# Optimization experiments

Hardware: AMD Instinct MI355X
Metric: run time of the kernel (lower is better)

## Reference

```python
import jax, jax.numpy as jnp
import numpy as np
from jax import lax

DN = ("NCDHW", "OIDHW", "NCDHW")


def bn(x, g, b, eps=1e-5):
    # torch BatchNorm3d training-mode forward: biased batch stats over (N, *, spatial)
    axes = (0,) + tuple(range(2, x.ndim))
    m = x.mean(axes, keepdims=True)
    v = x.var(axes, keepdims=True)
    shp = (1, -1) + (1,) * (x.ndim - 2)
    return (x - m) * lax.rsqrt(v + eps) * g.reshape(shp) + b.reshape(shp)


def conv_bn_relu(x, w, g, b, stride=(1, 1, 1), pad=(1, 0, 0)):
    y = lax.conv_general_dilated(x, w, stride, [(p, p) for p in pad], dimension_numbers=DN)
    return jax.nn.relu(bn(y, g, b))


def pw_bn_relu(x, w, g, b):  # 1x1x1 conv (no bias) + BN + ReLU on (B,C,T,H,W)
    y = jnp.einsum('oi,bithw->bothw', w, x)
    return jax.nn.relu(bn(y, g, b))


def pam_enc(x, pe_w, pe_g, pe_b):
    b, c, t, h, w = x.shape
    xm = x.mean(axis=2)  # all adaptive pools have T_out = 1
    feats = []
    for i, s in enumerate((1, 2, 3, 6)):  # H,W chosen divisible by 1,2,3,6 -> exact block means
        p = xm.reshape(b, c, s, h // s, s, w // s).mean(axis=(3, 5))  # (B,C,s,s)
        f = jnp.einsum('oi,bihw->bohw', pe_w[i], p)
        f = jax.nn.relu(bn(f, pe_g[i], pe_b[i]))
        feats.append(f.reshape(b, c, s * s))
    return jnp.concatenate(feats, axis=2)  # (B, C, 1+4+9+36=50)


def pam_dec(x, y, wq, bq, wk, bk, wv, bv, scale):
    # x: (B,C,T,H,W), y: (B,K,C)
    b, c, t, h, w = x.shape
    n = t * h * w
    q = jnp.einsum('oi,bithw->bothw', wq, x) + bq.reshape(1, -1, 1, 1, 1)
    q = q.reshape(b, c // 4, n).transpose(0, 2, 1)            # (B,N,C/4)
    k = y @ wk.T + bk                                         # (B,K,C/4)
    attn = jax.nn.softmax(jnp.einsum('bnd,bkd->bnk', q, k), axis=-1)
    v = y @ wv.T + bv                                         # (B,K,C)
    out = jnp.einsum('bkc,bnk->bcn', v, attn).reshape(b, c, t, h, w)
    return scale * out + x


def cam_dec(x, y, scale):
    b, c, t, h, w = x.shape
    xf = x.reshape(b, c, -1)
    yf = y.reshape(b, y.shape[1], -1)
    energy = jnp.einsum('bcn,bkn->bck', xf, yf)               # (B,C,K)
    attn = jax.nn.softmax(energy.max(-1, keepdims=True) - energy, axis=-1)
    out = jnp.einsum('bck,bkn->bcn', attn, yf).reshape(b, c, t, h, w)
    return x + scale * out


def tam_dec(x, y, scale):
    xp = x.transpose(0, 2, 1, 3, 4)  # (B,T,C,H,W)
    yp = y.transpose(0, 2, 1, 3, 4)
    b, t, c, h, w = xp.shape
    xf = xp.reshape(b, t, -1)
    yf = yp.reshape(b, t, -1)
    energy = jnp.einsum('bim,bjm->bij', xf, yf)               # (B,T,T)
    attn = jax.nn.softmax(energy.max(-1, keepdims=True) - energy, axis=-1)
    out = jnp.einsum('bij,bjm->bim', attn, yf).reshape(b, t, c, h, w)
    return (xp + scale * out).transpose(0, 2, 1, 3, 4)


def caf(x1, x2, w_conv1, g_conv1, b_conv1, w_conv2, g_conv2, b_conv2, w_tam, g_tam, b_tam, w_cat, g_cat, b_cat, pe_w, pe_g, pe_b, pd_wq, pd_bq, pd_wk, pd_bk, pd_wv, pd_bv, pd_scale, ce_w, ce_g, ce_b, cd_scale, te_w, te_g, te_b, td_scale):
    c1 = lambda z: conv_bn_relu(z, w_conv1, g_conv1, b_conv1)
    c2 = lambda z: conv_bn_relu(z, w_conv2, g_conv2, b_conv2)
    x1i = c1(x1)  # conv1(x1) is used by both PAM and CAM branches (identical in torch)
    x2i = c1(x2)
    # PAM branches
    x1_pa = c2(pam_dec(x1i, pam_enc(x1i, pe_w, pe_g, pe_b).transpose(0, 2, 1), pd_wq, pd_bq, pd_wk, pd_bk, pd_wv, pd_bv, pd_scale))
    x2_pa = c2(pam_dec(x2i, pam_enc(x2i, pe_w, pe_g, pe_b).transpose(0, 2, 1), pd_wq, pd_bq, pd_wk, pd_bk, pd_wv, pd_bv, pd_scale))
    # CAM branches
    x1_ca = c2(cam_dec(x1i, pw_bn_relu(x1i, ce_w, ce_g, ce_b), cd_scale))
    x2_ca = c2(cam_dec(x2i, pw_bn_relu(x2i, ce_w, ce_g, ce_b), cd_scale))
    # TAM branch over temporal concat (2T frames)
    xt1 = c1(jnp.concatenate([x1, x2], axis=2))
    xt2 = pw_bn_relu(xt1, te_w, te_g, te_b)
    x_ta = conv_bn_relu(tam_dec(xt1, xt2, td_scale), w_tam, g_tam, b_tam, stride=(2, 1, 1))
    out1 = conv_bn_relu(jnp.concatenate([x1_pa, x2_ca, x_ta], axis=1), w_cat, g_cat, b_cat)
    out2 = conv_bn_relu(jnp.concatenate([x2_pa, x1_ca, x_ta], axis=1), w_cat, g_cat, b_cat)
    return out1, out2


def setup_inputs() -> dict:
    key = jax.random.key(0)
    B, C, T, H, W = 4, 256, 16, 36, 36
    IC = C // 4
    ks = iter(jax.random.split(key, 24))
    rn = lambda shape, s=0.05: jax.random.normal(next(ks), shape, jnp.float32) * s
    ones = lambda n: jnp.ones((n,), jnp.float32)
    zeros = lambda n: jnp.zeros((n,), jnp.float32)
    return {
        "x1": rn((B, C, T, H, W), 1.0),
        "x2": rn((B, C, T, H, W), 1.0),
        "w_conv1": rn((IC, C, 3, 1, 1)), "g_conv1": ones(IC), "b_conv1": zeros(IC),
        "w_conv2": rn((IC, IC, 3, 1, 1)), "g_conv2": ones(IC), "b_conv2": zeros(IC),
        "w_tam": rn((IC, IC, 3, 1, 1)), "g_tam": ones(IC), "b_tam": zeros(IC),
        "w_cat": rn((C, 3 * IC, 3, 1, 1)), "g_cat": ones(C), "b_cat": zeros(C),
        "pe_w": rn((4, IC, IC)), "pe_g": jnp.ones((4, IC), jnp.float32), "pe_b": jnp.zeros((4, IC), jnp.float32),
        "pd_wq": rn((IC // 4, IC)), "pd_bq": zeros(IC // 4),
        "pd_wk": rn((IC // 4, IC)), "pd_bk": zeros(IC // 4),
        "pd_wv": rn((IC, IC)), "pd_bv": zeros(IC),
        "pd_scale": jnp.full((1,), 0.1, jnp.float32),
        "ce_w": rn((IC // 16, IC)), "ce_g": ones(IC // 16), "ce_b": zeros(IC // 16),
        "cd_scale": jnp.full((1,), 0.1, jnp.float32),
        "te_w": rn((IC, IC)), "te_g": ones(IC), "te_b": zeros(IC),
        "td_scale": jnp.full((1,), 0.1, jnp.float32),
    }


def reference(x1, x2, w_conv1, g_conv1, b_conv1, w_conv2, g_conv2, b_conv2, w_tam, g_tam, b_tam, w_cat, g_cat, b_cat, pe_w, pe_g, pe_b, pd_wq, pd_bq, pd_wk, pd_bk, pd_wv, pd_bv, pd_scale, ce_w, ce_g, ce_b, cd_scale, te_w, te_g, te_b, td_scale):
    return caf(x1, x2, w_conv1, g_conv1, b_conv1, w_conv2, g_conv2, b_conv2, w_tam, g_tam, b_tam, w_cat, g_cat, b_cat, pe_w, pe_g, pe_b, pd_wq, pd_bq, pd_wk, pd_bk, pd_wv, pd_bv, pd_scale, ce_w, ce_g, ce_b, cd_scale, te_w, te_g, te_b, td_scale)
```

## Files before the change

### kernel.cpp

```cpp
#include <hip/hip_runtime.h>

#define HW 1296
#define Nn 20736
#define N2 41472
#define TAPAD 72

typedef short bf16x8 __attribute__((ext_vector_type(8)));
typedef float f32x4 __attribute__((ext_vector_type(4)));

__device__ inline unsigned short f2b(float f){
  union { float f; unsigned u; } v; v.f = f;
  unsigned r = v.u + 0x7FFF + ((v.u >> 16) & 1);
  return (unsigned short)(r >> 16);
}
__device__ inline float b2f(unsigned short u){
  union { unsigned u; float f; } v; v.u = ((unsigned)u) << 16; return v.f;
}
__device__ inline float b2f_lo(unsigned u){
  union { unsigned u; float f; } v; v.u = u << 16; return v.f;
}
__device__ inline float b2f_hi(unsigned u){
  union { unsigned u; float f; } v; v.u = u & 0xffff0000u; return v.f;
}

__device__ __forceinline__ void pack_pairs(const float* a, unsigned* vals){
  #pragma unroll
  for (int i = 0; i < 32; ++i)
    vals[i] = (unsigned)f2b(a[2*i]) | ((unsigned)f2b(a[2*i+1]) << 16);
}

__device__ __forceinline__ void staged_write(unsigned* lds, int tid, const unsigned* vals,
                                             uint4* o4, size_t R0, int rowu4, int cw,
                                             uint4* o4b){
  #pragma unroll
  for (int i = 0; i < 32; ++i) lds[tid*33 + i] = vals[i];
  __syncthreads();
  #pragma unroll
  for (int k = 0; k < 8; ++k){
    int j = k*256 + tid;
    int nn = j >> 3, w = j & 7;
    int base = nn*33 + w*4;
    uint4 v;
    v.x = lds[base]; v.y = lds[base+1]; v.z = lds[base+2]; v.w = lds[base+3];
    size_t oidx = (R0 + (size_t)nn)*(size_t)rowu4 + cw + w;
    o4[oidx] = v;
    if (o4b) o4b[oidx] = v;
  }
  __syncthreads();
}


__global__ void k_zero(float* p, int n){
  int i = blockIdx.x*blockDim.x + threadIdx.x;
  if (i < n) p[i] = 0.f;
}

__device__ __forceinline__ void wpack_one(int e, const float* w, unsigned short* wp,
                                          int Cout, int Cin, int KT){
  int Kt32 = (Cin*KT) >> 5;
  int j    = e & 7;
  int lane = (e >> 3) & 63;
  int rest = e >> 9;
  int ks   = rest % Kt32;
  int mt   = rest / Kt32;
  int m  = mt*16 + (lane & 15);
  int k  = ks*32 + (lane >> 4)*8 + j;
  int dt = k / Cin, ci = k - dt*Cin;
  wp[e] = f2b(w[((size_t)m*Cin + ci)*KT + dt]);
}

__global__ void k_wprep(const float* w1, const float* w2, const float* wt,
                        const float* wc, const float* wte, const float* wce,
                        unsigned short* Wp1, unsigned short* Wp2, unsigned short* Wpt,
                        unsigned short* Wpc, unsigned short* Wpte, float* wTce){
  int idx = blockIdx.x*256 + threadIdx.x;
  if (idx < 49152){ wpack_one(idx, w1, Wp1, 64, 256, 3); return; }
  idx -= 49152;
  if (idx < 12288){ wpack_one(idx, w2, Wp2, 64, 64, 3); return; }
  idx -= 12288;
  if (idx < 12288){ wpack_one(idx, wt, Wpt, 64, 64, 3); return; }
  idx -= 12288;
  if (idx < 147456){ wpack_one(idx, wc, Wpc, 256, 192, 3); return; }
  idx -= 147456;
  if (idx < 4096){ wpack_one(idx, wte, Wpte, 64, 64, 1); return; }
  idx -= 4096;
  if (idx < 256){
    int o = idx / 64, i = idx % 64;
    wTce[i*4 + o] = wce[idx];
  }
}

__global__ void k_convT(const float* __restrict__ x1, const float* __restrict__ x2,
                        unsigned short* __restrict__ Pb){
  __shared__ unsigned lds[8448];
  int tid = threadIdx.x, z = blockIdx.z;
  int b = z & 3;
  const float* x = (z < 4) ? x1 : x2;
  int p0 = (z < 4) ? 0 : 16;
  int n0 = blockIdx.x*256, n = n0 + tid;
  const float* xb = x + (size_t)b*256*Nn + n;
  size_t R0 = (size_t)(b*32 + p0)*1296 + n0;
  uint4* o4 = (uint4*)Pb;
  for (int c0 = 0; c0 < 256; c0 += 64){
    float a[64];
    #pragma unroll
    for (int c = 0; c < 64; ++c) a[c] = xb[(size_t)(c0 + c)*Nn];
    unsigned vals[32];
    pack_pairs(a, vals);
    staged_write(lds, tid, vals, o4, R0, 32, c0 >> 3, nullptr);
  }
}

__device__ __forceinline__ void mf_body(const unsigned short* __restrict__ P,
                                        const unsigned short* __restrict__ Wp,
                                        void* __restrict__ out, float* __restrict__ sums,
                                        float* sredf,
                                        int Cin, int Cout, int mz, int b,
                                        int Tout, int stride, int KT, int pad,
                                        int p0, int plo, int phi, int PT, int obf)
{
  int lane = threadIdx.x & 63;
  int wave = threadIdx.x >> 6;
  int tile = blockIdx.x*4 + wave;
  bool valid = (tile < 27);
  int t = blockIdx.y;
  int col = lane & 15, grp = lane >> 4;
  int Kt32 = (KT*Cin) >> 5;
  f32x4 acc[4][3];
  #pragma unroll
  for (int i = 0; i < 4; ++i)
    #pragma unroll
    for (int j = 0; j < 3; ++j) acc[i][j] = (f32x4){0.f, 0.f, 0.f, 0.f};
  if (valid){
    int hw0 = tile*48 + col;
    const unsigned short* wbase = Wp + ((size_t)(mz*4)*Kt32)*512 + lane*8;
    for (int dt = 0; dt < KT; ++dt){
      int p = t*stride + dt - pad + p0;
      if (p < plo || p >= phi) continue;
      const unsigned short* Pp = P + ((size_t)(b*PT + p)*1296 + hw0)*Cin + grp*8;
      int nCk = Cin >> 5;
      int ksg = (dt*Cin) >> 5;
      for (int kc = 0; kc < nCk; ++kc){
        bf16x8 bf0 = *(const bf16x8*)(Pp + (size_t)0*Cin  + kc*32);
        bf16x8 bf1 = *(const bf16x8*)(Pp + (size_t)16*Cin + kc*32);
        bf16x8 bf2 = *(const bf16x8*)(Pp + (size_t)32*Cin + kc*32);
        #pragma unroll
        for (int mf = 0; mf < 4; ++mf){
          bf16x8 af = *(const bf16x8*)(wbase + ((size_t)mf*Kt32 + ksg + kc)*512);
          acc[mf][0] = __builtin_amdgcn_mfma_f32_16x16x32_bf16(af, bf0, acc[mf][0], 0, 0, 0);
          acc[mf][1] = __builtin_amdgcn_mfma_f32_16x16x32_bf16(af, bf1, acc[mf][1], 0, 0, 0);
          acc[mf][2] = __builtin_amdgcn_mfma_f32_16x16x32_bf16(af, bf2, acc[mf][2], 0, 0, 0);
        }
      }
    }
    size_t cs = (size_t)Tout*1296;
    size_t obase = ((size_t)(b*Cout + mz*64 + grp*4))*cs + (size_t)t*1296;
    if (obf){
      unsigned short* o16 = (unsigned short*)out;
      #pragma unroll
      for (int mf = 0; mf < 4; ++mf)
        #pragma unroll
        for (int f = 0; f < 3; ++f){
          int hw = tile*48 + f*16 + col;
          #pragma unroll
          for (int r = 0; r < 4; ++r)
            o16[obase + (size_t)(mf*16 + r)*cs + hw] = f2b(acc[mf][f][r]);
        }
    } else {
      float* o32 = (float*)out;
      #pragma unroll
      for (int mf = 0; mf < 4; ++mf)
        #pragma unroll
        for (int f = 0; f < 3; ++f){
          int hw = tile*48 + f*16 + col;
          #pragma unroll
          for (int r = 0; r < 4; ++r)
            o32[obase + (size_t)(mf*16 + r)*cs + hw] = acc[mf][f][r];
        }
    }
  }
  float s[16], q[16];
  #pragma unroll
  for (int mf = 0; mf < 4; ++mf)
    #pragma unroll
    for (int r = 0; r < 4; ++r){
      float v0 = acc[mf][0][r], v1 = acc[mf][1][r], v2 = acc[mf][2][r];
      s[mf*4+r] = v0 + v1 + v2;
      q[mf*4+r] = v0*v0 + v1*v1 + v2*v2;
    }
  #pragma unroll
  for (int m = 1; m <= 8; m <<= 1){
    #pragma unroll
    for (int j = 0; j < 16; ++j){
      s[j] += __shfl_xor(s[j], m);
      q[j] += __shfl_xor(q[j], m);
    }
  }
  if (col == 0){
    #pragma unroll
    for (int j = 0; j < 16; ++j){
      sredf[((0*4 + wave)*4 + grp)*16 + j] = s[j];
      sredf[((1*4 + wave)*4 + grp)*16 + j] = q[j];
    }
  }
  __syncthreads();
  int tid = threadIdx.x;
  if (tid < 128){
    int stat = tid >> 6, ch = tid & 63;
    int rr = ch & 3, gg = (ch >> 2) & 3, mm = ch >> 4;
    int j = mm*4 + rr;
    float v = sredf[((stat*4 + 0)*4 + gg)*16 + j] + sredf[((stat*4 + 1)*4 + gg)*16 + j]
            + sredf[((stat*4 + 2)*4 + gg)*16 + j] + sredf[((stat*4 + 3)*4 + gg)*16 + j];
    atomicAdd(&sums[stat*Cout + mz*64 + ch], v);
  }
}

__launch_bounds__(256)
__global__ void k_mfconv(const unsigned short* __restrict__ P, const unsigned short* __restrict__ Wp,
                         float* __restrict__ out, int Cin, int Cout, int Mz,
                         int Tout, int stride, int KT, int pad, int p0, int plo, int phi, int PT,
                         float* __restrict__ sums, int obf)
{
  __shared__ float sred[2*4*4*16];
  int bz = blockIdx.z; int b = bz / Mz; int mz = bz - b*Mz;
  mf_body(P, Wp, out, sums, sred, Cin, Cout, mz, b, Tout, stride, KT, pad,
          p0, plo, phi, PT, obf);
}

__launch_bounds__(256)
__global__ void k_mfconv_ab(const unsigned short* __restrict__ P, const unsigned short* __restrict__ Wp,
                            float* __restrict__ A, float* __restrict__ Bb,
                            float* __restrict__ stats)
{
  __shared__ float sred[2*4*4*16];
  int bz = blockIdx.z; int which = bz >> 2; int b = bz & 3;
  float* out = which ? Bb : A;
  float* sums = stats + (size_t)which*512;
  int p0 = which*16;
  mf_body(P, Wp, out, sums, sred, 256, 64, 0, b, 16, 1, 3, 1, p0, p0, p0+16, 32, 0);
}

__launch_bounds__(256)
__global__ void k_mfconv4(const unsigned short* __restrict__ PG4, const unsigned short* __restrict__ Wp,
                          unsigned short* __restrict__ Rout, float* __restrict__ stats)
{
  __shared__ float sred[2*4*4*16];
  int pb = blockIdx.z;
  int stage = pb >> 2;
  int slot = (stage < 2) ? (13 + stage) : (15 + stage);
  mf_body(PG4, Wp, Rout, stats + (size_t)slot*512, sred, 64, 64, 0, pb,
          16, 1, 3, 1, 0, 0, 16, 16, 1);
}

__launch_bounds__(256)
__global__ void k_mfconvcat(const unsigned short* __restrict__ PCAT1, const unsigned short* __restrict__ PCAT2,
                            const unsigned short* __restrict__ Wp,
                            unsigned short* __restrict__ CATR1, unsigned short* __restrict__ CATR2,
                            float* __restrict__ stats)
{
  __shared__ float sred[2*4*4*16];
  int bz = blockIdx.z;
  int which = bz >> 4; int rem = bz & 15;
  int b = rem >> 2; int mz = rem & 3;
  const unsigned short* P = which ? PCAT2 : PCAT1;
  unsigned short* out = which ? CATR2 : CATR1;
  float* sums = stats + (size_t)(19 + which)*512;
  mf_body(P, Wp, out, sums, sred, 192, 256, mz, b, 16, 1, 3, 1, 0, 0, 16, 16, 1);
}

__global__ void k_tconvm(const float* __restrict__ A, const float* __restrict__ Bb,
                         const float* __restrict__ wT,
                         float* __restrict__ yc2, float* __restrict__ stats)
{
  __shared__ float r1[4][64], r2[4][64];
  int z = blockIdx.z;
  int which = z >> 2, b = z & 3;
  const float* xA = which ? Bb : A;
  float* out = yc2 + (size_t)which*331776;
  float* sums = stats + (size_t)(15 + which)*512;
  int o  = threadIdx.x;
  int ty = threadIdx.y;
  int t  = blockIdx.y;
  int hw4 = blockIdx.x*64 + ty;
  bool valid = (hw4 < 324);
  float4 acc = make_float4(0.f,0.f,0.f,0.f);
  if (valid){
    const float4* xr = (const float4*)xA + ((size_t)b*64*16 + t)*324 + hw4;
    const float* wp  = wT + o;
    size_t xstep = (size_t)16*324;
    for (int i = 0; i < 64; ++i){
      float4 xv = *xr;
      float  wv = *wp;
      acc.x = fmaf(wv, xv.x, acc.x);
      acc.y = fmaf(wv, xv.y, acc.y);
      acc.z = fmaf(wv, xv.z, acc.z);
      acc.w = fmaf(wv, xv.w, acc.w);
      xr += xstep; wp += 4;
    }
    float4* op = (float4*)out + ((size_t)(b*4 + o)*16 + t)*324 + hw4;
    *op = acc;
  }
  r1[o][ty] = acc.x + acc.y + acc.z + acc.w;
  r2[o][ty] = acc.x*acc.x + acc.y*acc.y + acc.z*acc.z + acc.w*acc.w;
  __syncthreads();
  int tid = threadIdx.y*4 + threadIdx.x;
  for (int k = 32; k > 0; k >>= 1){
    if (ty < k){
      r1[o][ty] += r1[o][ty+k];
      r2[o][ty] += r2[o][ty+k];
    }
    __syncthreads();
  }
  if (tid < 4) atomicAdd(&sums[tid],     r1[tid][0]);
  else if (tid < 8) atomicAdd(&sums[tid], r2[tid-4][0]);
}


__global__ void k_planestats(const float* __restrict__ A, const float* __restrict__ B,
                             float* __restrict__ s22, float* __restrict__ s23){
  int which = blockIdx.z, c = blockIdx.y, tid = threadIdx.x;
  const float* src = which ? B : A;
  int toff = which ? 0 : 15;
  float* dst = which ? s23 : s22;
  float s = 0.f, q = 0.f;
  for (int idx = tid; idx < 4*1296; idx += 256){
    int b = idx / 1296, hw = idx - b*1296;
    float v = src[(((size_t)b*64 + c)*16 + toff)*1296 + hw];
    s += v; q += v*v;
  }
  __shared__ float r1[256], r2[256];
  r1[tid] = s; r2[tid] = q; __syncthreads();
  for (int k = 128; k > 0; k >>= 1){
    if (tid < k){ r1[tid] += r1[tid+k]; r2[tid] += r2[tid+k]; }
    __syncthreads();
  }
  if (tid == 0){ dst[c] = r1[0]; dst[64 + c] = r2[0]; }
}

__global__ void k_combine(float* stats){
  int i = threadIdx.x;
  if (i < 128)
    stats[2*512 + i] = stats[0*512 + i] + stats[1*512 + i]
                     - stats[22*512 + i] - stats[23*512 + i] + stats[21*512 + i];
}

__global__ void k_bnrelu_out(const unsigned short* __restrict__ x1bf,
                             const unsigned short* __restrict__ x2bf,
                             const float* __restrict__ stats19,
                             const float* __restrict__ g,
                             const float* __restrict__ bet, float invc,
                             float* __restrict__ out)
{
  int z = blockIdx.z;
  int b = z & 3, which = z >> 2;
  const unsigned short* xbf = which ? x2bf : x1bf;
  const float* sums = stats19 + (size_t)which*512;
  float* op = out + (size_t)which*4*256*Nn;
  int c = blockIdx.y;
  int n8 = blockIdx.x*256 + threadIdx.x;
  if (n8 >= 2592) return;
  float m  = sums[c]*invc;
  float v  = fmaxf(sums[256+c]*invc - m*m, 0.f);
  float sc = g[c]*rsqrtf(v + 1e-5f);
  float bb = bet[c] - m*sc;
  size_t base = ((size_t)(b*256 + c))*Nn + (size_t)n8*8;
  uint4 u = *(const uint4*)(xbf + base);
  float4 o0, o1;
  o0.x = fmaxf(fmaf(b2f_lo(u.x), sc, bb), 0.f);
  o0.y = fmaxf(fmaf(b2f_hi(u.x), sc, bb), 0.f);
  o0.z = fmaxf(fmaf(b2f_lo(u.y), sc, bb), 0.f);
  o0.w = fmaxf(fmaf(b2f_hi(u.y), sc, bb), 0.f);
  o1.x = fmaxf(fmaf(b2f_lo(u.z), sc, bb), 0.f);
  o1.y = fmaxf(fmaf(b2f_hi(u.z), sc, bb), 0.f);
  o1.z = fmaxf(fmaf(b2f_lo(u.w), sc, bb), 0.f);
  o1.w = fmaxf(fmaf(b2f_hi(u.w), sc, bb), 0.f);
  *(float4*)(op + base) = o0;
  *(float4*)(op + base + 4) = o1;
}

__global__ void k_bnrelu_mean2(float* __restrict__ A, float* __restrict__ Bb,
                               const float* __restrict__ stats,
                               const float* __restrict__ g, const float* __restrict__ bet,
                               float invc, float* __restrict__ p6a, float* __restrict__ p6b)
{
  __shared__ float p6loc[36];
  int z = blockIdx.z;
  int which = z >> 2, b = z & 3;
  float* x = which ? Bb : A;
  const float* sums = stats + (size_t)which*512;
  float* p6 = which ? p6b : p6a;
  int tid = threadIdx.x;
  if (tid < 36) p6loc[tid] = 0.f;
  __syncthreads();
  int hw = blockIdx.x*256 + tid;
  int c = blockIdx.y;
  if (hw < 1296){
    float m  = sums[c]*invc;
    float v  = fmaxf(sums[64+c]*invc - m*m, 0.f);
    float sc = g[c]*rsqrtf(v + 1e-5f);
    float bb = bet[c] - m*sc;
    float* xb = x + ((size_t)(b*64 + c)*16)*1296 + hw;
    float s = 0.f;
    #pragma unroll
    for (int t = 0; t < 16; ++t){
      float val = fmaxf(fmaf(xb[(size_t)t*1296], sc, bb), 0.f);
      xb[(size_t)t*1296] = val;
      s += val;
    }
    int h = hw / 36, w = hw - h*36;
    atomicAdd(&p6loc[(h/6)*6 + (w/6)], s*(1.f/16.f));
  }
  __syncthreads();
  if (tid < 36) atomicAdd(&p6[((size_t)(b*64 + c))*36 + tid], p6loc[tid]);
}

__global__ void k_bnT(const void* __restrict__ xraw, const float* __restrict__ sums,
                      const float* __restrict__ g, const float* __restrict__ bet, float invc,
                      unsigned short* __restrict__ P1, unsigned short* __restrict__ P2,
                      int L, int outC, int coff, int xbf)
{
  __shared__ unsigned lds[8448];
  int tid = threadIdx.x, b = blockIdx.z;
  int n0 = blockIdx.x*256, n = n0 + tid;
  float a[64];
  if (xbf){
    const unsigned short* xb = (const unsigned short*)xraw + (size_t)b*64*L + n;
    #pragma unroll
    for (int c = 0; c < 64; ++c){
      float m  = sums[c]*invc;
      float vv = fmaxf(sums[64+c]*invc - m*m, 0.f);
      float sc = g[c]*rsqrtf(vv + 1e-5f);
      float bb = bet[c] - m*sc;
      a[c] = fmaxf(fmaf(b2f(xb[(size_t)c*L]), sc, bb), 0.f);
    }
  } else {
    const float* xb = (const float*)xraw + (size_t)b*64*L + n;
    #pragma unroll
    for (int c = 0; c < 64; ++c){
      float m  = sums[c]*invc;
      float vv = fmaxf(sums[64+c]*invc - m*m, 0.f);
      float sc = g[c]*rsqrtf(vv + 1e-5f);
      float bb = bet[c] - m*sc;
      a[c] = fmaxf(fmaf(xb[(size_t)c*L], sc, bb), 0.f);
    }
  }
  unsigned vals[32];
  pack_pairs(a, vals);
  staged_write(lds, tid, vals, (uint4*)P1, (size_t)b*L + n0, outC >> 3, coff >> 3,
               P2 ? (uint4*)P2 : nullptr);
}

__global__ void k_bnT4(const unsigned short* __restrict__ R4, const float* __restrict__ stats,
                       const float* __restrict__ g, const float* __restrict__ bet, float invc,
                       unsigned short* __restrict__ PCAT1, unsigned short* __restrict__ PCAT2)
{
  __shared__ unsigned lds[8448];
  int z = blockIdx.z;
  int stage = z >> 2, b = z & 3;
  int slot = (stage < 2) ? (13 + stage) : (15 + stage);
  const float* sums = stats + (size_t)slot*512;
  unsigned short* P1 = (stage == 0 || stage == 3) ? PCAT1 : PCAT2;
  int cw = (stage < 2) ? 0 : 8;
  int tid = threadIdx.x;
  int n0 = blockIdx.x*256, n = n0 + tid;
  const unsigned short* xb = R4 + (size_t)z*64*Nn + n;
  float a[64];
  #pragma unroll
  for (int c = 0; c < 64; ++c){
    float m  = sums[c]*invc;
    float vv = fmaxf(sums[64+c]*invc - m*m, 0.f);
    float sc = g[c]*rsqrtf(vv + 1e-5f);
    float bb = bet[c] - m*sc;
    a[c] = fmaxf(fmaf(b2f(xb[(size_t)c*Nn]), sc, bb), 0.f);
  }
  unsigned vals[32];
  pack_pairs(a, vals);
  staged_write(lds, tid, vals, (uint4*)P1, (size_t)b*Nn + n0, 24, cw, nullptr);
}

__global__ void k_bnT_cc(const float* __restrict__ A, const float* __restrict__ M,
                         const float* __restrict__ B, const float* __restrict__ sums,
                         const float* __restrict__ g, const float* __restrict__ bet,
                         float invc, unsigned short* __restrict__ P1)
{
  __shared__ unsigned lds[8448];
  int tid = threadIdx.x, b = blockIdx.z;
  int n0 = blockIdx.x*256, n = n0 + tid;
  int t = n / 1296, hw = n - t*1296;
  const float* src; size_t cstride;
  if (t < 15){ src = A + ((size_t)(b*64)*16 + t)*1296 + hw; cstride = (size_t)16*1296; }
  else if (t < 17){ src = M + ((size_t)(b*64)*2 + (t-15))*1296 + hw; cstride = (size_t)2*1296; }
  else { src = B + ((size_t)(b*64)*16 + (t-16))*1296 + hw; cstride = (size_t)16*1296; }
  float a[64];
  #pragma unroll
  for (int c = 0; c < 64; ++c){
    float m  = sums[c]*invc;
    float vv = fmaxf(sums[64+c]*invc - m*m, 0.f);
    float sc = g[c]*rsqrtf(vv + 1e-5f);
    float bb = bet[c] - m*sc;
    a[c] = fmaxf(fmaf(src[c*cstride], sc, bb), 0.f);
  }
  unsigned vals[32];
  pack_pairs(a, vals);
  staged_write(lds, tid, vals, (uint4*)P1, (size_t)b*N2 + n0, 8, 0, nullptr);
}


__global__ void k_pamenc1m(const float* __restrict__ p6a, const float* __restrict__ p6b,
                           const float* __restrict__ pe_w,
                           float* __restrict__ pf2, float* __restrict__ stats){
  __shared__ float psh[64];
  int z = blockIdx.z;
  int which = z >> 2, b = z & 3;
  const float* p6 = which ? p6b : p6a;
  float* sl = stats + (size_t)(which ? 9 : 5)*512;
  float* pf = pf2 + (size_t)which*12800;
  int cell = blockIdx.x;
  int o = threadIdx.x;
  int s, off;
  if (cell < 1){ s=1; off=0; } else if (cell < 5){ s=2; off=1; }
  else if (cell < 14){ s=3; off=5; } else { s=6; off=14; }
  int local = cell - off, ph = local/s, pw = local%s;
  int bs = 6/s;
  const float* pp = p6 + ((size_t)(b*64 + o))*36;
  float sum = 0.f;
  for (int i = 0; i < bs; ++i)
    for (int j = 0; j < bs; ++j)
      sum += pp[(ph*bs + i)*6 + (pw*bs + j)];
  psh[o] = sum * ((float)(s*s) * (1.f/1296.f));
  __syncthreads();
  int grp = (cell < 1) ? 0 : (cell < 5) ? 1 : (cell < 14) ? 2 : 3;
  const float* w = pe_w + (size_t)grp*4096 + o*64;
  float acc = 0.f;
  #pragma unroll
  for (int i = 0; i < 64; ++i) acc = fmaf(w[i], psh[i], acc);
  pf[((size_t)b*64 + o)*50 + cell] = acc;
  atomicAdd(&sl[grp*128 + o], acc);
  atomicAdd(&sl[grp*128 + 64 + o], acc*acc);
}

__launch_bounds__(128)
__global__ void k_pamenc2m(const float* __restrict__ pf2, float* __restrict__ stats,
                           const float* __restrict__ pe_g, const float* __restrict__ pe_b,
                           const float* __restrict__ wk, const float* __restrict__ bk,
                           const float* __restrict__ wv, const float* __restrict__ bv,
                           const float* __restrict__ wq, const float* __restrict__ bq,
                           float* __restrict__ vb2, float* __restrict__ KW2,
                           float* __restrict__ sb2)
{
  __shared__ float yk[64];
  __shared__ float kbl[16];
  int z = blockIdx.z;
  int which = z >> 2, b = z & 3;
  const float* pf = pf2 + (size_t)which*12800;
  const float* sl = stats + (size_t)(which ? 9 : 5)*512;
  float* vb = vb2 + (size_t)which*12800;
  float* KW = KW2 + (size_t)which*12800;
  float* sb = sb2 + (size_t)which*256;
  int k = blockIdx.x;
  int tid = threadIdx.x;
  int grp = (k < 1) ? 0 : (k < 5) ? 1 : (k < 14) ? 2 : 3;
  const float ss2[4] = {1.f, 4.f, 9.f, 36.f};
  if (tid < 64){
    float invc = 1.f/(4.f*ss2[grp]);
    float m = sl[grp*128 + tid]*invc;
    float var = fmaxf(sl[grp*128 + 64 + tid]*invc - m*m, 0.f);
    float sc = pe_g[grp*64 + tid]*rsqrtf(var + 1e-5f);
    float sh = pe_b[grp*64 + tid] - m*sc;
    yk[tid] = fmaxf(fmaf(pf[((size_t)b*64 + tid)*50 + k], sc, sh), 0.f);
  }
  __syncthreads();
  if (tid < 16){
    float s = bk[tid];
    #pragma unroll
    for (int c = 0; c < 64; ++c) s = fmaf(wk[tid*64 + c], yk[c], s);
    kbl[tid] = s;
  } else if (tid < 80){
    int c = tid - 16;
    float s = bv[c];
    #pragma unroll
    for (int i = 0; i < 64; ++i) s = fmaf(wv[c*64 + i], yk[i], s);
    vb[((size_t)b*50 + k)*64 + c] = s;
  }
  __syncthreads();
  if (tid < 64){
    float s = 0.f;
    #pragma unroll
    for (int o = 0; o < 16; ++o) s = fmaf(kbl[o], wq[o*64 + tid], s);
    KW[((size_t)b*50 + k)*64 + tid] = s;
  } else if (tid == 64){
    float s = 0.f;
    #pragma unroll
    for (int o = 0; o < 16; ++o) s = fmaf(kbl[o], bq[o], s);
    sb[(size_t)b*50 + k] = s;
  }
}

__launch_bounds__(256, 1)
__global__ void k_pamattnm(const float* __restrict__ A, const float* __restrict__ Bb,
                           const float* __restrict__ KW2, const float* __restrict__ sb2,
                           const float* __restrict__ vb2, const float* __restrict__ scp,
                           unsigned short* __restrict__ PG4)
{
  __shared__ unsigned smem_u[8448];
  float* smem = (float*)smem_u;
  int z = blockIdx.z;
  int which = z >> 2, b = z & 3;
  const float* x = which ? Bb : A;
  const float* KW = KW2 + (size_t)which*12800;
  const float* sbb = sb2 + (size_t)which*256;
  const float* vbuf = vb2 + (size_t)which*12800;
  int tid = threadIdx.x;
  for (int i = tid; i < 3200; i += 256){
    smem[i]        = KW[(size_t)b*3200 + i];
    smem[3200 + i] = vbuf[(size_t)b*3200 + i];
  }
  if (tid < 50) smem[6400 + tid] = sbb[(size_t)b*50 + tid];
  __syncthreads();
  int n0 = blockIdx.x*256;
  int n = n0 + tid;
  const float* xb = x + (size_t)b*64*Nn + n;
  float xv[64];
  #pragma unroll
  for (int c = 0; c < 64; ++c) xv[c] = xb[(size_t)c*Nn];
  float s[50];
  const float4* kw4 = (const float4*)smem;
  #pragma unroll
  for (int k = 0; k < 50; ++k){
    float t = smem[6400 + k];
    #pragma unroll
    for (int c4 = 0; c4 < 16; ++c4){
      float4 kw = kw4[k*16 + c4];
      t = fmaf(xv[c4*4+0], kw.x, t);
      t = fmaf(xv[c4*4+1], kw.y, t);
      t = fmaf(xv[c4*4+2], kw.z, t);
      t = fmaf(xv[c4*4+3], kw.w, t);
    }
    s[k] = t;
  }
  float mx = -1e30f;
  #pragma unroll
  for (int k = 0; k < 50; ++k) mx = fmaxf(mx, s[k]);
  float sum = 0.f;
  #pragma unroll
  for (int k = 0; k < 50; ++k){ float p = __expf(s[k]-mx); s[k] = p; sum += p; }
  float sc = scp[0]/sum;
  const float4* vl4 = (const float4*)(smem + 3200);
  #pragma unroll
  for (int k = 0; k < 50; ++k){
    float pk = sc * s[k];
    #pragma unroll
    for (int c4 = 0; c4 < 16; ++c4){
      float4 v = vl4[k*16 + c4];
      xv[c4*4+0] = fmaf(pk, v.x, xv[c4*4+0]);
      xv[c4*4+1] = fmaf(pk, v.y, xv[c4*4+1]);
      xv[c4*4+2] = fmaf(pk, v.z, xv[c4*4+2]);
      xv[c4*4+3] = fmaf(pk, v.w, xv[c4*4+3]);
    }
  }
  __syncthreads();
  unsigned vals[32];
  pack_pairs(xv, vals);
  staged_write(smem_u, tid, vals, (uint4*)PG4, (size_t)(which*4 + b)*Nn + n0, 8, 0, nullptr);
}


__global__ void k_camenergy2m(const float* __restrict__ A, const float* __restrict__ Bb,
                              const float* __restrict__ yc2, const float* __restrict__ stats,
                              const float* __restrict__ ce_g, const float* __restrict__ ce_b,
                              float invc, float* __restrict__ e_cam){
  __shared__ float yl[4][256];
  int z = blockIdx.z;
  int which = z >> 2, b = z & 3;
  const float* x = which ? Bb : A;
  const float* yc = yc2 + (size_t)which*331776;
  const float* sums = stats + (size_t)(15 + which)*512;
  float* e = e_cam + (size_t)which*1024;
  int tid = threadIdx.x;
  int n0 = blockIdx.x*256;
  #pragma unroll
  for (int k = 0; k < 4; ++k){
    float m  = sums[k]*invc;
    float vv = fmaxf(sums[4+k]*invc - m*m, 0.f);
    float sck = ce_g[k]*rsqrtf(vv + 1e-5f);
    float bbk = ce_b[k] - m*sck;
    float raw = yc[((size_t)b*4+k)*Nn + n0 + tid];
    yl[k][tid] = fmaxf(fmaf(raw, sck, bbk), 0.f);
  }
  __syncthreads();
  int c = tid & 63, ks = tid >> 6;
  const float* xr = x + (size_t)(b*64+c)*Nn + n0;
  const float* yr = yl[ks];
  float acc = 0.f;
  #pragma unroll 8
  for (int i = 0; i < 256; ++i) acc = fmaf(xr[i], yr[i], acc);
  atomicAdd(&e[((size_t)(b*64)+c)*4 + ks], acc);
}

__global__ void k_camapplyTm(const float* __restrict__ A, const float* __restrict__ Bb,
                             const float* __restrict__ yc2, const float* __restrict__ stats,
                             const float* __restrict__ ce_g, const float* __restrict__ ce_b,
                             float invc, const float* __restrict__ e_cam,
                             const float* __restrict__ scp, unsigned short* __restrict__ PG4){
  __shared__ float pw[64][4];
  __shared__ unsigned lds[8448];
  int z = blockIdx.z;
  int which = z >> 2, b = z & 3;
  const float* x = which ? Bb : A;
  const float* yc = yc2 + (size_t)which*331776;
  const float* sums = stats + (size_t)(15 + which)*512;
  const float* e = e_cam + (size_t)which*1024;
  int tid = threadIdx.x;
  if (tid < 64){
    const float* er = e + (size_t)(b*64+tid)*4;
    float e0=er[0], e1=er[1], e2=er[2], e3=er[3];
    float mx = fmaxf(fmaxf(e0,e1), fmaxf(e2,e3));
    float z0=mx-e0, z1=mx-e1, z2=mx-e2, z3=mx-e3;
    float zm = fmaxf(fmaxf(z0,z1), fmaxf(z2,z3));
    float p0=__expf(z0-zm), p1=__expf(z1-zm), p2=__expf(z2-zm), p3=__expf(z3-zm);
    float inv = 1.f/(p0+p1+p2+p3);
    pw[tid][0]=p0*inv; pw[tid][1]=p1*inv; pw[tid][2]=p2*inv; pw[tid][3]=p3*inv;
  }
  __syncthreads();
  int n0 = blockIdx.x*256;
  int n = n0 + tid;
  float yv[4];
  #pragma unroll
  for (int k = 0; k < 4; ++k){
    float m  = sums[k]*invc;
    float vv = fmaxf(sums[4+k]*invc - m*m, 0.f);
    float sck = ce_g[k]*rsqrtf(vv + 1e-5f);
    float bbk = ce_b[k] - m*sck;
    yv[k] = fmaxf(fmaf(yc[((size_t)b*4+k)*Nn + n], sck, bbk), 0.f);
  }
  float sc = scp[0];
  const float* xb = x + (size_t)b*64*Nn + n;
  float a[64];
  #pragma unroll
  for (int c = 0; c < 64; ++c){
    a[c] = fmaf(sc, pw[c][0]*yv[0] + pw[c][1]*yv[1] + pw[c][2]*yv[2] + pw[c][3]*yv[3],
                xb[(size_t)c*Nn]);
  }
  unsigned vals[32];
  pack_pairs(a, vals);
  staged_write(lds, tid, vals, (uint4*)PG4, (size_t)((2+which)*4 + b)*Nn + n0, 8, 0, nullptr);
}


__launch_bounds__(256)
__global__ void k_tamenergy_mf(const unsigned short* __restrict__ X,
                               const unsigned short* __restrict__ Y,
                               float* __restrict__ E){
  int b = blockIdx.z;
  int wave = threadIdx.x >> 6, lane = threadIdx.x & 63;
  int r = lane & 15, g = lane >> 4;
  const unsigned short* Xb = X + (size_t)b*32*82944;
  const unsigned short* Yb = Y + (size_t)b*32*82944;
  f32x4 a00 = (f32x4){0.f,0.f,0.f,0.f};
  f32x4 a01 = a00, a10 = a00, a11 = a00;
  int c0 = (blockIdx.x*4 + wave)*8;
  for (int cc = 0; cc < 8; ++cc){
    size_t k0 = (size_t)(c0 + cc)*32 + (size_t)g*8;
    bf16x8 x0 = *(const bf16x8*)(Xb + (size_t)r*82944 + k0);
    bf16x8 x1 = *(const bf16x8*)(Xb + (size_t)(r+16)*82944 + k0);
    bf16x8 y0 = *(const bf16x8*)(Yb + (size_t)r*82944 + k0);
    bf16x8 y1 = *(const bf16x8*)(Yb + (size_t)(r+16)*82944 + k0);
    a00 = __builtin_amdgcn_mfma_f32_16x16x32_bf16(x0, y0, a00, 0, 0, 0);
    a01 = __builtin_amdgcn_mfma_f32_16x16x32_bf16(x0, y1, a01, 0, 0, 0);
    a10 = __builtin_amdgcn_mfma_f32_16x16x32_bf16(x1, y0, a10, 0, 0, 0);
    a11 = __builtin_amdgcn_mfma_f32_16x16x32_bf16(x1, y1, a11, 0, 0, 0);
  }
  float* Eb = E + (size_t)b*1024;
  #pragma unroll
  for (int rr = 0; rr < 4; ++rr){
    int row = g*4 + rr;
    atomicAdd(&Eb[row*32 + r],           a00[rr]);
    atomicAdd(&Eb[row*32 + 16 + r],      a01[rr]);
    atomicAdd(&Eb[(row+16)*32 + r],      a10[rr]);
    atomicAdd(&Eb[(row+16)*32 + 16 + r], a11[rr]);
  }
}

__launch_bounds__(256)
__global__ void k_tamapply_mf(const unsigned short* __restrict__ Xbf,
                              const unsigned short* __restrict__ Ybf,
                              const float* __restrict__ e, const float* __restrict__ scp,
                              unsigned short* __restrict__ Pout){
  __shared__ unsigned short yl[32*8*TAPAD];
  __shared__ float al[1024];
  int b = blockIdx.z, tid = threadIdx.x;
  int hw0 = blockIdx.x*8;
  if (tid < 32){
    const float* er = e + (size_t)b*1024 + tid*32;
    float mx = -1e30f, mn = 1e30f;
    for (int j = 0; j < 32; ++j){ mx = fmaxf(mx, er[j]); mn = fminf(mn, er[j]); }
    float zmax = mx - mn;
    float sum = 0.f;
    for (int j = 0; j < 32; ++j){
      float p = __expf((mx - er[j]) - zmax);
      al[tid*32 + j] = p; sum += p;
    }
    float inv = 1.f/sum;
    for (int j = 0; j < 32; ++j) al[tid*32 + j] *= inv;
  }
  const uint4* src = (const uint4*)Ybf + (size_t)b*N2*8;
  #pragma unroll
  for (int it = 0; it < 8; ++it){
    int idx = it*256 + tid;
    int j = idx >> 6, rem = idx & 63, h = rem >> 3, w = rem & 7;
    uint4 v = src[(size_t)(j*1296 + hw0 + h)*8 + w];
    *(uint4*)&yl[(j*8+h)*TAPAD + w*8] = v;
  }
  __syncthreads();
  int t = tid >> 3, h = tid & 7;
  int n = t*1296 + hw0 + h;
  float sc = scp[0];
  const uint4* xr = (const uint4*)Xbf + ((size_t)b*N2 + n)*8;
  float acc[64];
  #pragma unroll
  for (int w = 0; w < 8; ++w){
    uint4 v = xr[w];
    acc[w*8+0] = b2f_lo(v.x); acc[w*8+1] = b2f_hi(v.x);
    acc[w*8+2] = b2f_lo(v.y); acc[w*8+3] = b2f_hi(v.y);
    acc[w*8+4] = b2f_lo(v.z); acc[w*8+5] = b2f_hi(v.z);
    acc[w*8+6] = b2f_lo(v.w); acc[w*8+7] = b2f_hi(v.w);
  }
  const float* ar = &al[t*32];
  for (int j = 0; j < 32; ++j){
    float aj = sc * ar[j];
    const uint4* yr = (const uint4*)&yl[(j*8+h)*TAPAD];
    #pragma unroll
    for (int w = 0; w < 8; ++w){
      uint4 v = yr[w];
      acc[w*8+0] = fmaf(aj, b2f_lo(v.x), acc[w*8+0]);
      acc[w*8+1] = fmaf(aj, b2f_hi(v.x), acc[w*8+1]);
      acc[w*8+2] = fmaf(aj, b2f_lo(v.y), acc[w*8+2]);
      acc[w*8+3] = fmaf(aj, b2f_hi(v.y), acc[w*8+3]);
      acc[w*8+4] = fmaf(aj, b2f_lo(v.z), acc[w*8+4]);
      acc[w*8+5] = fmaf(aj, b2f_hi(v.z), acc[w*8+5]);
      acc[w*8+6] = fmaf(aj, b2f_lo(v.w), acc[w*8+6]);
      acc[w*8+7] = fmaf(aj, b2f_hi(v.w), acc[w*8+7]);
    }
  }
  uint4* orow = (uint4*)Pout + ((size_t)b*N2 + n)*8;
  #pragma unroll
  for (int w = 0; w < 8; ++w){
    uint4 v;
    v.x = (unsigned)f2b(acc[w*8+0]) | ((unsigned)f2b(acc[w*8+1]) << 16);
    v.y = (unsigned)f2b(acc[w*8+2]) | ((unsigned)f2b(acc[w*8+3]) << 16);
    v.z = (unsigned)f2b(acc[w*8+4]) | ((unsigned)f2b(acc[w*8+5]) << 16);
    v.w = (unsigned)f2b(acc[w*8+6]) | ((unsigned)f2b(acc[w*8+7]) << 16);
    orow[w] = v;
  }
}


extern "C" void kernel_launch(void* const* d_in, const int* in_sizes, int n_in,
                              void* d_out, int out_size, void* d_ws, size_t ws_size,
                              hipStream_t stream) {
  const float* x1      = (const float*)d_in[0];
  const float* x2      = (const float*)d_in[1];
  const float* w_conv1 = (const float*)d_in[2];
  const float* g_conv1 = (const float*)d_in[3];
  const float* b_conv1 = (const float*)d_in[4];
  const float* w_conv2 = (const float*)d_in[5];
  const float* g_conv2 = (const float*)d_in[6];
  const float* b_conv2 = (const float*)d_in[7];
  const float* w_tam   = (const float*)d_in[8];
  const float* g_tam   = (const float*)d_in[9];
  const float* b_tam   = (const float*)d_in[10];
  const float* w_cat   = (const float*)d_in[11];
  const float* g_cat   = (const float*)d_in[12];
  const float* b_cat   = (const float*)d_in[13];
  const float* pe_w    = (const float*)d_in[14];
  const float* pe_g    = (const float*)d_in[15];
  const float* pe_b    = (const float*)d_in[16];
  const float* pd_wq   = (const float*)d_in[17];
  const float* pd_bq   = (const float*)d_in[18];
  const float* pd_wk   = (const float*)d_in[19];
  const float* pd_bk   = (const float*)d_in[20];
  const float* pd_wv   = (const float*)d_in[21];
  const float* pd_bv   = (const float*)d_in[22];
  const float* pd_scale= (const float*)d_in[23];
  const float* ce_w    = (const float*)d_in[24];
  const float* ce_g    = (const float*)d_in[25];
  const float* ce_b    = (const float*)d_in[26];
  const float* cd_scale= (const float*)d_in[27];
  const float* te_w    = (const float*)d_in[28];
  const float* te_g    = (const float*)d_in[29];
  const float* te_b    = (const float*)d_in[30];
  const float* td_scale= (const float*)d_in[31];

  float* ws = (float*)d_ws;
  size_t off = 0;
  auto alloc = [&](size_t n){ float* p = ws + off; off += (n + 3) & ~(size_t)3; return p; };
  float* stats = alloc(16384);
  float* e_tam = alloc(4096);
  float* e_cam = alloc(2048);
  float* p6a   = alloc(9216);
  float* p6b   = alloc(9216);
  float* wTce  = alloc(256);
  unsigned short* Wp1  = (unsigned short*)alloc(24576);
  unsigned short* Wp2  = (unsigned short*)alloc(6144);
  unsigned short* Wpt  = (unsigned short*)alloc(6144);
  unsigned short* Wpc  = (unsigned short*)alloc(73728);
  unsigned short* Wpte = (unsigned short*)alloc(2048);
  float* pf2   = alloc(25600);
  float* vb2   = alloc(25600);
  float* KW2   = alloc(25600);
  float* sb2   = alloc(512);
  float* yc2   = alloc(663552);
  float* Mb    = alloc(663552);
  float* A     = alloc(5308416);
  float* Bb    = alloc(5308416);
  float* PTEf  = alloc(5308416);
  float* COMB  = alloc(31850496);

  unsigned short* P0 = (unsigned short*)COMB;
  unsigned short* DdBF = (unsigned short*)COMB;
  unsigned short* Dbf  = (unsigned short*)(COMB + 10616832);
  unsigned short* PTAM = (unsigned short*)(COMB + 15925248);
  unsigned short* RrawBF = (unsigned short*)COMB;
  unsigned short* PCAT1 = (unsigned short*)(COMB + 5308416);
  unsigned short* PCAT2 = (unsigned short*)(COMB + 13271040);
  unsigned short* PG4   = (unsigned short*)(COMB + 21233664);
  unsigned short* R4    = (unsigned short*)A;
  unsigned short* CATR1 = (unsigned short*)(COMB + 21233664);
  unsigned short* CATR2 = (unsigned short*)A;
  unsigned short* PTE = (unsigned short*)PTEf;

  const float invc16 = 1.f/(4.f*20736.f);
  const float invc32 = 1.f/(4.f*41472.f);

  k_zero<<<dim3(160), 256, 0, stream>>>(stats, 40960);
  k_wprep<<<dim3(881), 256, 0, stream>>>(w_conv1, w_conv2, w_tam, w_cat, te_w, ce_w,
                                         Wp1, Wp2, Wpt, Wpc, Wpte, wTce);
  k_convT<<<dim3(81, 1, 8), 256, 0, stream>>>(x1, x2, P0);

  k_mfconv_ab<<<dim3(7,16,8), 256, 0, stream>>>(P0, Wp1, A, Bb, stats);
  k_mfconv<<<dim3(7,2,4), 256, 0, stream>>>(P0, Wp1, Mb, 256, 64, 1, 2, 1, 3, 1, 15, 0, 32, 32, stats + 21*512, 0);
  k_planestats<<<dim3(1,64,2), 256, 0, stream>>>(A, Bb, stats + 22*512, stats + 23*512);
  k_combine<<<dim3(1), 128, 0, stream>>>(stats);
  k_bnT_cc<<<dim3(162,1,4), 256, 0, stream>>>(A, Mb, Bb, stats + 2*512,
                                              g_conv1, b_conv1, invc32, PTE);

  k_mfconv<<<dim3(7,32,4), 256, 0, stream>>>(PTE, Wpte, (float*)DdBF, 64, 64, 1, 32, 1, 1, 0, 0, 0, 32, 32, stats + 3*512, 1);
  k_bnT<<<dim3(162,1,4), 256, 0, stream>>>(DdBF, stats + 3*512, te_g, te_b, invc32,
                                           Dbf, nullptr, N2, 64, 0, 1);

  k_tamenergy_mf<<<dim3(81, 1, 4), 256, 0, stream>>>(PTE, Dbf, e_tam);
  k_tamapply_mf<<<dim3(162, 1, 4), 256, 0, stream>>>(PTE, Dbf, e_tam, td_scale, PTAM);
  k_mfconv<<<dim3(7,16,4), 256, 0, stream>>>(PTAM, Wpt, (float*)RrawBF, 64, 64, 1, 16, 2, 3, 1, 0, 0, 32, 32, stats + 4*512, 1);
  k_bnT<<<dim3(81,1,4), 256, 0, stream>>>(RrawBF, stats + 4*512, g_tam, b_tam, invc16,
                                          PCAT1, PCAT2, Nn, 192, 128, 1);

  k_bnrelu_mean2<<<dim3(6,64,8), 256, 0, stream>>>(A, Bb, stats, g_conv1, b_conv1,
                                                   invc16, p6a, p6b);
  k_pamenc1m<<<dim3(50,1,8), 64, 0, stream>>>(p6a, p6b, pe_w, pf2, stats);
  k_pamenc2m<<<dim3(50,1,8), 128, 0, stream>>>(pf2, stats, pe_g, pe_b,
                                               pd_wk, pd_bk, pd_wv, pd_bv, pd_wq, pd_bq,
                                               vb2, KW2, sb2);
  k_pamattnm<<<dim3(81,1,8), 256, 0, stream>>>(A, Bb, KW2, sb2, vb2, pd_scale, PG4);
  k_tconvm<<<dim3(6,16,8), dim3(4,64), 0, stream>>>(A, Bb, wTce, yc2, stats);
  k_camenergy2m<<<dim3(81,1,8), 256, 0, stream>>>(A, Bb, yc2, stats, ce_g, ce_b,
                                                  invc16, e_cam);
  k_camapplyTm<<<dim3(81,1,8), 256, 0, stream>>>(A, Bb, yc2, stats, ce_g, ce_b,
                                                 invc16, e_cam, cd_scale, PG4);

  k_mfconv4<<<dim3(7,16,16), 256, 0, stream>>>(PG4, Wp2, R4, stats);
  k_bnT4<<<dim3(81,1,16), 256, 0, stream>>>(R4, stats, g_conv2, b_conv2, invc16,
                                            PCAT1, PCAT2);

  k_mfconvcat<<<dim3(7,16,32), 256, 0, stream>>>(PCAT1, PCAT2, Wpc, CATR1, CATR2, stats);
  k_bnrelu_out<<<dim3(11, 256, 8), 256, 0, stream>>>(CATR1, CATR2, stats + 19*512,
                                                     g_cat, b_cat, invc16, (float*)d_out);
}
```

Measured before the change: 742.5 us.

## Replace generic MFMA concat conv with specialized direct-register kernel

Replaces the generic mf_body-based concat temporal conv with a dedicated kernel. Each block covers a 48-pixel tile, and its four waves each compute 64 output channels. Operands are loaded straight from global memory into MFMA fragments with no shared-memory staging. BN statistics are reduced with wave shuffles before the atomics. The goal is less generic-path overhead and LDS traffic, at the cost of relying on L1/L2 for input reuse across the four waves and uncoalesced bf16 output stores.

Result: slower. 931.3 us (+25.4%).

```diff
diff --git a/kernel.cpp b/kernel.cpp
--- a/kernel.cpp
+++ b/kernel.cpp
@@ -253,19 +253,87 @@
 }
 
 __launch_bounds__(256)
-__global__ void k_mfconvcat(const unsigned short* __restrict__ PCAT1, const unsigned short* __restrict__ PCAT2,
-                            const unsigned short* __restrict__ Wp,
-                            unsigned short* __restrict__ CATR1, unsigned short* __restrict__ CATR2,
-                            float* __restrict__ stats)
-{
-  __shared__ float sred[2*4*4*16];
-  int bz = blockIdx.z;
-  int which = bz >> 4; int rem = bz & 15;
-  int b = rem >> 2; int mz = rem & 3;
+__global__ void k_mfconvcat2(const unsigned short* __restrict__ PCAT1,
+                             const unsigned short* __restrict__ PCAT2,
+                             const unsigned short* __restrict__ Wp,
+                             unsigned short* __restrict__ CATR1,
+                             unsigned short* __restrict__ CATR2,
+                             float* __restrict__ stats)
+{
+  const int Cin = 192, Cout = 256, Tout = 16, PT = 16;
+  int z = blockIdx.z;
+  int which = z >> 2, b = z & 3;
   const unsigned short* P = which ? PCAT2 : PCAT1;
   unsigned short* out = which ? CATR2 : CATR1;
   float* sums = stats + (size_t)(19 + which)*512;
-  mf_body(P, Wp, out, sums, sred, 192, 256, mz, b, 16, 1, 3, 1, 0, 0, 16, 16, 1);
+  int lane = threadIdx.x & 63;
+  int mz = threadIdx.x >> 6;
+  int tile = blockIdx.x;
+  int t = blockIdx.y;
+  int col = lane & 15, grp = lane >> 4;
+  const int Kt32 = (3*Cin) >> 5;
+  f32x4 acc[4][3];
+  #pragma unroll
+  for (int i = 0; i < 4; ++i)
+    #pragma unroll
+    for (int j = 0; j < 3; ++j) acc[i][j] = (f32x4){0.f, 0.f, 0.f, 0.f};
+  int hw0 = tile*48 + col;
+  const unsigned short* wbase = Wp + ((size_t)(mz*4)*Kt32)*512 + lane*8;
+  for (int dt = 0; dt < 3; ++dt){
+    int p = t + dt - 1;
+    if (p < 0 || p >= 16) continue;
+    const unsigned short* Pp = P + ((size_t)(b*PT + p)*1296 + hw0)*Cin + grp*8;
+    int ksg = (dt*Cin) >> 5;
+    for (int kc = 0; kc < 6; ++kc){
+      bf16x8 bf0 = *(const bf16x8*)(Pp + (size_t)0*Cin  + kc*32);
+      bf16x8 bf1 = *(const bf16x8*)(Pp + (size_t)16*Cin + kc*32);
+      bf16x8 bf2 = *(const bf16x8*)(Pp + (size_t)32*Cin + kc*32);
+      #pragma unroll
+      for (int mf = 0; mf < 4; ++mf){
+        bf16x8 af = *(const bf16x8*)(wbase + ((size_t)mf*Kt32 + ksg + kc)*512);
+        acc[mf][0] = __builtin_amdgcn_mfma_f32_16x16x32_bf16(af, bf0, acc[mf][0], 0, 0, 0);
+        acc[mf][1] = __builtin_amdgcn_mfma_f32_16x16x32_bf16(af, bf1, acc[mf][1], 0, 0, 0);
+        acc[mf][2] = __builtin_amdgcn_mfma_f32_16x16x32_bf16(af, bf2, acc[mf][2], 0, 0, 0);
+      }
+    }
+  }
+  size_t cs = (size_t)Tout*1296;
+  size_t obase = ((size_t)(b*Cout + mz*64 + grp*4))*cs + (size_t)t*1296;
+  #pragma unroll
+  for (int mf = 0; mf < 4; ++mf)
+    #pragma unroll
+    for (int f = 0; f < 3; ++f){
+      int hw = tile*48 + f*16 + col;
+      #pragma unroll
+      for (int r = 0; r < 4; ++r)
+        out[obase + (size_t)(mf*16 + r)*cs + hw] = f2b(acc[mf][f][r]);
+    }
+  float s[16], q[16];
+  #pragma unroll
+  for (int mf = 0; mf < 4; ++mf)
+    #pragma unroll
+    for (int r = 0; r < 4; ++r){
+      float v0 = acc[mf][0][r], v1 = acc[mf][1][r], v2 = acc[mf][2][r];
+      s[mf*4+r] = v0 + v1 + v2;
+      q[mf*4+r] = v0*v0 + v1*v1 + v2*v2;
+    }
+  #pragma unroll
+  for (int m = 1; m <= 8; m <<= 1){
+    #pragma unroll
+    for (int j = 0; j < 16; ++j){
+      s[j] += __shfl_xor(s[j], m);
+      q[j] += __shfl_xor(q[j], m);
+    }
+  }
+  if (col == 0){
+    #pragma unroll
+    for (int j = 0; j < 16; ++j){
+      int mf = j >> 2, r = j & 3;
+      int ch = mz*64 + mf*16 + grp*4 + r;
+      atomicAdd(&sums[ch], s[j]);
+      atomicAdd(&sums[256 + ch], q[j]);
+    }
+  }
 }
 
 __global__ void k_tconvm(const float* __restrict__ A, const float* __restrict__ Bb,
@@ -971,7 +1039,7 @@
   k_bnT4<<<dim3(81,1,16), 256, 0, stream>>>(R4, stats, g_conv2, b_conv2, invc16,
                                             PCAT1, PCAT2);
 
-  k_mfconvcat<<<dim3(7,16,32), 256, 0, stream>>>(PCAT1, PCAT2, Wpc, CATR1, CATR2, stats);
+  k_mfconvcat2<<<dim3(27,16,8), 256, 0, stream>>>(PCAT1, PCAT2, Wpc, CATR1, CATR2, stats);
   k_bnrelu_out<<<dim3(11, 256, 8), 256, 0, stream>>>(CATR1, CATR2, stats + 19*512,
                                                      g_cat, b_cat, invc16, (float*)d_out);
 }
```
